# Performance work log

Measured on AMD Instinct MI355X. Metric: run time of the kernel, lower is better.

The kernel has to match this reference:

```python
import jax, jax.numpy as jnp
import numpy as np
from jax import lax

# Graph / problem sizes (a realistic chain denominator FST)
T, B, D = 150, 64, 2000   # frames, batch, num_pdfs
S, E = 3000, 100000       # FST states, FST arcs


def setup_inputs() -> dict:
    key = jax.random.key(0)
    k0, k1, k2, k3, k4, k5, k6 = jax.random.split(key, 7)
    inp = jax.random.normal(k0, (T, B, D), dtype=jnp.float32)          # nnet log-prob outputs
    from_state = jax.random.randint(k1, (E,), 0, S, dtype=jnp.int32)
    to_state = jax.random.randint(k2, (E,), 0, S, dtype=jnp.int32)
    pdf_id = jax.random.randint(k3, (E,), 0, D, dtype=jnp.int32)
    trans_logw = jax.random.normal(k4, (E,), dtype=jnp.float32) * 0.1 - 2.0  # arc log-weights
    init_logp = jax.random.normal(k5, (S,), dtype=jnp.float32) * 0.1 - np.log(S).astype(np.float32)
    final_logp = jax.random.normal(k6, (S,), dtype=jnp.float32) * 0.1 - 1.0
    return {
        "input": inp,
        "trans_logw": trans_logw,
        "init_logp": init_logp,
        "final_logp": final_logp,
        "from_state": from_state,
        "to_state": to_state,
        "pdf_id": pdf_id,
    }


def _logsumexp_scatter(scores, seg, num_segments):
    """Stable log-sum-exp of `scores` ([E, B]) scattered into segments along axis 0."""
    m = jax.ops.segment_max(scores, seg, num_segments=num_segments)      # [S, B]
    m_safe = jnp.where(jnp.isfinite(m), m, 0.0)
    s = jax.ops.segment_sum(jnp.exp(scores - m_safe[seg]), seg,
                            num_segments=num_segments)                   # [S, B]
    return jnp.where(s > 0, m_safe + jnp.log(s), -jnp.inf)


def reference(input, trans_logw, init_logp, final_logp, from_state, to_state, pdf_id):
    # Log-domain forward recursion over the denominator FST (LF-MMI denominator objf).
    # alpha: [S, B] log forward scores per state per sequence.
    num_states = init_logp.shape[0]
    alpha0 = jnp.broadcast_to(init_logp[:, None], (num_states, input.shape[1]))

    def step(alpha, x_t):
        # x_t: [B, D]. Arc score = alpha[src] + arc weight + emission log-prob of arc's pdf.
        scores = alpha[from_state] + trans_logw[:, None] + x_t.T[pdf_id]   # [E, B]
        alpha_next = _logsumexp_scatter(scores, to_state, num_states)      # [S, B]
        return alpha_next, None

    alpha_T, _ = lax.scan(step, alpha0, input)
    # Total log-likelihood: sum over batch of logsumexp over final states.
    objf = jnp.sum(jax.scipy.special.logsumexp(alpha_T + final_logp[:, None], axis=0))
    return objf
```

## Files before the change

### kernel.cpp

```cpp
#include <hip/hip_runtime.h>
#include <math.h>

#define TT 150
#define BB 64
#define DD 2000
#define SS 3000
#define EE 100000
#define EEPAD 124160
#define RESC 16
#define NSLOT 9
#define RESCC 0x1p-46f

#define NT 1024
#define NBLK 256
#define NG 16
#define GB 16
#define CAP 8192
#define ASTRD 3072
#define NSTMAX 1024
#define FLGSTR 32
#define NEXB 32
#define EXCH 125

#define OFF_ALPHA  0
#define OFF_EX     24064
#define OFF_ARC    40192
#define OFF_RBP    105728
#define OFF_SORD   109840
#define OFF_RED    113936
#define OFF_SH     118032
#define OFF_LSP    118048
#define DYNLDS     118128

struct __align__(8) ArcT2 { unsigned idx; float ew; };

__device__ inline float b2f(unsigned short u) {
    union { unsigned u32; float f; } x; x.u32 = ((unsigned)u) << 16; return x.f;
}
__device__ inline unsigned short f2b(float f) {
    union { float f; unsigned u; } x; x.f = f;
    unsigned r = x.u + 0x7FFF + ((x.u >> 16) & 1);
    return (unsigned short)(r >> 16);
}
__device__ inline float u2f(unsigned u) {
    union { unsigned u32; float f; } x; x.u32 = u; return x.f;
}

template <int CTRL>
__device__ inline float dpp_add(float v) {
    int x = __builtin_amdgcn_update_dpp(0, __float_as_int(v), CTRL, 0xF, 0xF, true);
    return v + __int_as_float(x);
}

__global__ void k_init0(int* __restrict__ counts, unsigned* __restrict__ flags,
                        float* __restrict__ partial)
{
    int i = blockIdx.x * blockDim.x + threadIdx.x;
    if (i < SS) counts[i] = 0;
    if (i < 2 * NBLK * FLGSTR) flags[i] = 0u;
    if (i < NG * 4) partial[i] = 0.f;
}

__global__ void k_zeroarcs(ArcT2* __restrict__ arcs)
{
    int i = blockIdx.x * blockDim.x + threadIdx.x;
    if (i < EEPAD) { ArcT2 z; z.idx = 0; z.ew = 0.f; arcs[i] = z; }
}

__global__ void k_hist(const int* __restrict__ to_state, int* __restrict__ counts)
{
    int e = blockIdx.x * blockDim.x + threadIdx.x;
    if (e < EE) atomicAdd(&counts[to_state[e]], 1);
}

__global__ void k_scan(const int* __restrict__ counts, int* __restrict__ rp,
                       int* __restrict__ cur)
{
    __shared__ int ls[1024];
    int tid = threadIdx.x;
    int s0 = tid * 3;
    int a0 = (s0 + 0 < SS) ? ((counts[s0 + 0] + 7) & ~7) : 0;
    int a1 = (s0 + 1 < SS) ? ((counts[s0 + 1] + 7) & ~7) : 0;
    int a2 = (s0 + 2 < SS) ? ((counts[s0 + 2] + 7) & ~7) : 0;
    int tsum = a0 + a1 + a2;
    ls[tid] = tsum;
    __syncthreads();
    for (int off = 1; off < 1024; off <<= 1) {
        int v = ls[tid];
        int add = (tid >= off) ? ls[tid - off] : 0;
        __syncthreads();
        ls[tid] = v + add;
        __syncthreads();
    }
    int excl = ls[tid] - tsum;
    if (s0 + 0 < SS) { rp[s0 + 0] = excl; cur[s0 + 0] = excl; }
    excl += a0;
    if (s0 + 1 < SS) { rp[s0 + 1] = excl; cur[s0 + 1] = excl; }
    excl += a1;
    if (s0 + 2 < SS) { rp[s0 + 2] = excl; cur[s0 + 2] = excl; }
    if (tid == 1023) rp[SS] = ls[1023];
}

__global__ void k_split(const int* __restrict__ rp, int* __restrict__ split)
{
    int j = threadIdx.x;
    if (j > GB) return;
    if (j == 0)  { split[0] = 0; return; }
    if (j == GB) { split[GB] = SS; return; }
    long long total = rp[SS];
    int target = (int)((total * j) / GB);
    int lo = 0, hi = SS;
    while (lo < hi) { int mid = (lo + hi) >> 1; if (rp[mid] >= target) hi = mid; else lo = mid + 1; }
    split[j] = lo;
}

__global__ void k_sortst(const int* __restrict__ rp, const int* __restrict__ split,
                         int* __restrict__ sordg)
{
    __shared__ int hist[128];
    __shared__ int off[128];
    int j = blockIdx.x;
    int s0 = split[j], s1 = split[j + 1];
    int nst = s1 - s0; if (nst > NSTMAX) nst = NSTMAX;
    int tid = threadIdx.x;
    if (tid < 128) hist[tid] = 0;
    __syncthreads();
    for (int i = tid; i < nst; i += 256) {
        int nit = (rp[s0 + i + 1] - rp[s0 + i]) >> 2;
        if (nit > 127) nit = 127;
        atomicAdd(&hist[nit], 1);
    }
    __syncthreads();
    if (tid == 0) {
        int acc = 0;
        for (int b = 127; b >= 0; --b) { off[b] = acc; acc += hist[b]; }
    }
    __syncthreads();
    for (int i = tid; i < nst; i += 256) {
        int nit = (rp[s0 + i + 1] - rp[s0 + i]) >> 2;
        if (nit > 127) nit = 127;
        int pos = atomicAdd(&off[nit], 1);
        sordg[j * NSTMAX + pos] = i;
    }
}

__global__ void k_scatter(const int* __restrict__ from_state, const int* __restrict__ to_state,
                          const int* __restrict__ pdf_id, const float* __restrict__ trans_logw,
                          int* __restrict__ cur, ArcT2* __restrict__ arcs)
{
    int e = blockIdx.x * blockDim.x + threadIdx.x;
    if (e >= EE) return;
    int s = to_state[e];
    int pos = atomicAdd(&cur[s], 1);
    ArcT2 a;
    a.idx = ((unsigned)from_state[e] << 3) | ((unsigned)pdf_id[e] << 19);
    a.ew = __expf(trans_logw[e]);
    arcs[pos] = a;
}

__global__ void __launch_bounds__(NT, 4) k_coop(
    const ArcT2* __restrict__ arcs, const int* __restrict__ rp,
    const int* __restrict__ split, const int* __restrict__ sordg,
    const float* __restrict__ input, const float* __restrict__ init_logp,
    const float* __restrict__ final_logp,
    float* __restrict__ partial,
    unsigned long long* __restrict__ A_all,
    unsigned* __restrict__ flags,
    unsigned* __restrict__ xcdbuf,
    float* __restrict__ out)
{
    extern __shared__ char dsm[];
    unsigned long long* la64  = (unsigned long long*)(dsm + OFF_ALPHA);
    unsigned long long* lex64 = (unsigned long long*)(dsm + OFF_EX);
    ArcT2*    larc  = (ArcT2*)(dsm + OFF_ARC);
    int*      rbp   = (int*)(dsm + OFF_RBP);
    float*    redf  = (float*)(dsm + OFF_RED);
    int*      sh    = (int*)(dsm + OFF_SH);
    int*      sord  = (int*)(dsm + OFF_SORD);
    int*      lsp   = (int*)(dsm + OFF_LSP);

    int tid = threadIdx.x, bid = blockIdx.x;
    int x = bid & 7, y = (bid >> 3) & 1, j = bid >> 4;
    int g = x * 2 + y;
    int lane = tid & 63, wave = tid >> 6;
    int qid = lane >> 2, sub = lane & 3;

    unsigned long long* Ag = A_all + (size_t)g * (2 * ASTRD);
    unsigned* stepf    = flags;
    unsigned* auxf     = flags + (size_t)NBLK * FLGSTR;
    unsigned* myflag   = stepf + (size_t)(g * GB + j) * FLGSTR;
    unsigned* grpflag  = stepf + (size_t)(g * GB) * FLGSTR;
    unsigned* myflag2  = auxf + (size_t)(g * GB + j) * FLGSTR;
    unsigned* grpflag2 = auxf + (size_t)(g * GB) * FLGSTR;
    const float* inpG  = input + (size_t)(4 * g) * DD;

    int s0 = split[j], s1 = split[j + 1];
    int nst = s1 - s0;
    if (nst > NSTMAX) nst = NSTMAX;

    for (int i = tid; i <= nst; i += NT) rbp[i] = rp[s0 + i];
    for (int i = tid; i < nst; i += NT) sord[i] = sordg[j * NSTMAX + i];
    if (tid <= GB) lsp[tid] = split[tid];
    __syncthreads();
    int rb0 = rbp[0];
    {
        int staged = rbp[nst] - rb0; if (staged > CAP) staged = CAP;
        for (int i = tid; i < staged; i += NT) larc[i] = arcs[rb0 + i];
    }

    unsigned xcd = __builtin_amdgcn_s_getreg(6164) & 0xF;
    if (tid == 0)
        __hip_atomic_store(&xcdbuf[g * GB + j], xcd, __ATOMIC_RELAXED, __HIP_MEMORY_SCOPE_AGENT);
    __syncthreads();
    if (tid == 0)
        __hip_atomic_store(myflag2, 1u, __ATOMIC_RELAXED, __HIP_MEMORY_SCOPE_AGENT);
    if (wave == 0) {
        while (true) {
            unsigned ok = 1;
            #pragma unroll
            for (int r = 0; r < 4; ++r) {
                unsigned v = __hip_atomic_load(auxf + (size_t)(lane * 4 + r) * FLGSTR,
                                               __ATOMIC_RELAXED, __HIP_MEMORY_SCOPE_AGENT);
                ok &= (v >= 1u);
            }
            if (__ballot(ok != 0) == ~0ULL) break;
            __builtin_amdgcn_s_sleep(1);
        }
    }
    __syncthreads();
    {
        int* xint = (int*)redf;
        if (tid < NBLK)
            xint[tid] = (int)__hip_atomic_load(&xcdbuf[tid], __ATOMIC_RELAXED,
                                               __HIP_MEMORY_SCOPE_AGENT);
        __syncthreads();
        if (tid == 0) {
            int x0 = xint[g * GB];
            int uni = 1;
            for (int m = 1; m < GB; ++m) uni &= (xint[g * GB + m] == x0);
            int first = xint[0], distinct = 0;
            for (int i = 1; i < NBLK; ++i) distinct |= (xint[i] != first);
            sh[0] = uni && distinct;
        }
        __syncthreads();
    }
    const bool fast = (sh[0] != 0);
    __syncthreads();

    float pf[2][4];
    auto prefetch = [&](const float* fr) {
        int d0 = wave * EXCH;
        #pragma unroll
        for (int r = 0; r < 2; ++r) {
            int dd = r * 64 + lane;
            if (dd < EXCH) {
                int d = d0 + dd;
                #pragma unroll
                for (int c = 0; c < 4; ++c) pf[r][c] = fr[c * DD + d];
            }
        }
    };

    auto exchange = [&](unsigned epv, const unsigned long long* src64) {
        {
            int d0 = wave * EXCH;
            #pragma unroll
            for (int r = 0; r < 2; ++r) {
                int dd = r * 64 + lane;
                if (dd < EXCH) {
                    int d = d0 + dd;
                    unsigned w0 = (unsigned)f2b(__expf(pf[r][0])) |
                                  ((unsigned)f2b(__expf(pf[r][1])) << 16);
                    unsigned w1 = (unsigned)f2b(__expf(pf[r][2])) |
                                  ((unsigned)f2b(__expf(pf[r][3])) << 16);
                    lex64[d] = (unsigned long long)w0 | ((unsigned long long)w1 << 32);
                }
            }
        }
        int p = wave;
        const unsigned* gf = grpflag + (size_t)p * FLGSTR;
        if (fast) {
            while (*(volatile const unsigned*)gf < epv) { }
            int a = lsp[p], b = lsp[p + 1];
            for (int i = a + lane; i < b; i += 64)
                la64[i] = *(volatile const unsigned long long*)(src64 + i);
        } else {
            while (__hip_atomic_load(gf, __ATOMIC_RELAXED, __HIP_MEMORY_SCOPE_AGENT) < epv)
                __builtin_amdgcn_s_sleep(1);
            int a = lsp[p], b = lsp[p + 1];
            for (int i = a + lane; i < b; i += 64)
                la64[i] = __hip_atomic_load(src64 + i, __ATOMIC_RELAXED,
                                            __HIP_MEMORY_SCOPE_AGENT);
        }
    };

    prefetch(inpG);
    for (int i = tid; i < nst; i += NT) {
        int s = s0 + i;
        unsigned short h = f2b(__expf(init_logp[s]));
        unsigned w = (unsigned)h | ((unsigned)h << 16);
        unsigned long long pk = (unsigned long long)w | ((unsigned long long)w << 32);
        if (fast) Ag[s] = pk;
        else __hip_atomic_store(Ag + s, pk, __ATOMIC_RELAXED, __HIP_MEMORY_SCOPE_AGENT);
    }
    __syncthreads();
    unsigned ep = 1;
    if (tid == 0) {
        if (fast) *(volatile unsigned*)myflag = ep;
        else __hip_atomic_store(myflag, ep, __ATOMIC_RELAXED, __HIP_MEMORY_SCOPE_AGENT);
    }
    exchange(ep, Ag );
    __syncthreads();

    float vf0 = 0.f, vf1 = 0.f, vf2 = 0.f, vf3 = 0.f;

    for (int k = 0; k < TT; ++k) {
        unsigned long long* An64 = Ag + ((k + 1) & 1) * ASTRD;
        bool last = (k == TT - 1);
        bool resc = (((k + 1) & (RESC - 1)) == 0);

        if (!last) prefetch(inpG + (size_t)(k + 1) * BB * DD);

        for (int base = wave * 16; base < nst; base += 256) {
            int li = base + qid;
            bool has = (li < nst);
            float acc0 = 0.f, acc1 = 0.f, acc2 = 0.f, acc3 = 0.f;
            int sg = 0;
            if (has) {
                int so = sord[li];
                sg = s0 + so;
                int ra = rbp[so], re = rbp[so + 1];
                int nit = (re - ra) >> 2;
                if (re - rb0 <= CAP) {
                    int bix = ra - rb0 + sub;
                    for (int t = 0; t < nit; ++t) {
                        ArcT2 a = larc[bix + t * 4];
                        uint2 au = *(const uint2*)(dsm + (a.idx & 0xFFFFu));
                        uint2 eu = *(const uint2*)(dsm + OFF_EX + (a.idx >> 16));
                        acc0 = fmaf(u2f(au.x << 16), a.ew * u2f(eu.x << 16), acc0);
                        acc1 = fmaf(u2f(au.x & 0xFFFF0000u), a.ew * u2f(eu.x & 0xFFFF0000u), acc1);
                        acc2 = fmaf(u2f(au.y << 16), a.ew * u2f(eu.y << 16), acc2);
                        acc3 = fmaf(u2f(au.y & 0xFFFF0000u), a.ew * u2f(eu.y & 0xFFFF0000u), acc3);
                    }
                } else {
                    for (int t = 0; t < nit; ++t) {
                        ArcT2 a = arcs[ra + t * 4 + sub];
                        uint2 au = *(const uint2*)(dsm + (a.idx & 0xFFFFu));
                        uint2 eu = *(const uint2*)(dsm + OFF_EX + (a.idx >> 16));
                        acc0 = fmaf(u2f(au.x << 16), a.ew * u2f(eu.x << 16), acc0);
                        acc1 = fmaf(u2f(au.x & 0xFFFF0000u), a.ew * u2f(eu.x & 0xFFFF0000u), acc1);
                        acc2 = fmaf(u2f(au.y << 16), a.ew * u2f(eu.y << 16), acc2);
                        acc3 = fmaf(u2f(au.y & 0xFFFF0000u), a.ew * u2f(eu.y & 0xFFFF0000u), acc3);
                    }
                }
            }
            acc0 = dpp_add<0xB1>(acc0); acc1 = dpp_add<0xB1>(acc1);
            acc2 = dpp_add<0xB1>(acc2); acc3 = dpp_add<0xB1>(acc3);
            acc0 = dpp_add<0x4E>(acc0); acc1 = dpp_add<0x4E>(acc1);
            acc2 = dpp_add<0x4E>(acc2); acc3 = dpp_add<0x4E>(acc3);
            if (has && sub == 0) {
                if (resc) { acc0 *= RESCC; acc1 *= RESCC; acc2 *= RESCC; acc3 *= RESCC; }
                if (last) {
                    float ef = __expf(final_logp[sg]);
                    vf0 = fmaf(acc0, ef, vf0);
                    vf1 = fmaf(acc1, ef, vf1);
                    vf2 = fmaf(acc2, ef, vf2);
                    vf3 = fmaf(acc3, ef, vf3);
                } else {
                    unsigned w0 = (unsigned)f2b(acc0) | ((unsigned)f2b(acc1) << 16);
                    unsigned w1 = (unsigned)f2b(acc2) | ((unsigned)f2b(acc3) << 16);
                    unsigned long long pk = (unsigned long long)w0 |
                                            ((unsigned long long)w1 << 32);
                    if (fast) An64[sg] = pk;
                    else __hip_atomic_store(An64 + sg, pk, __ATOMIC_RELAXED,
                                            __HIP_MEMORY_SCOPE_AGENT);
                }
            }
        }
        if (last) break;
        __syncthreads();
        ++ep;
        if (tid == 0) {
            if (fast) *(volatile unsigned*)myflag = ep;
            else __hip_atomic_store(myflag, ep, __ATOMIC_RELAXED, __HIP_MEMORY_SCOPE_AGENT);
        }
        exchange(ep, An64);
        __syncthreads();
    }

    if (sub == 0) {
        int r0 = (wave * 16 + qid) * 4;
        redf[r0 + 0] = vf0; redf[r0 + 1] = vf1;
        redf[r0 + 2] = vf2; redf[r0 + 3] = vf3;
    }
    __syncthreads();
    if (tid < 4) {
        float S = 0.f;
        for (int i = 0; i < 256; ++i) S += redf[i * 4 + tid];
        __hip_atomic_fetch_add(&partial[g * 4 + tid], S, __ATOMIC_RELAXED,
                               __HIP_MEMORY_SCOPE_AGENT);
    }
    __syncthreads();
    if (tid == 0)
        __hip_atomic_store(myflag2, 2u, __ATOMIC_RELAXED, __HIP_MEMORY_SCOPE_AGENT);
    if (j == 0) {
        if (wave == 0) {
            while (true) {
                unsigned v = 2;
                if (lane < GB)
                    v = __hip_atomic_load(grpflag2 + lane * FLGSTR, __ATOMIC_RELAXED,
                                          __HIP_MEMORY_SCOPE_AGENT);
                if (__ballot(v >= 2) == ~0ULL) break;
                __builtin_amdgcn_s_sleep(1);
            }
        }
        __syncthreads();
        if (tid < 4) {
            float S = __hip_atomic_load(&partial[g * 4 + tid], __ATOMIC_RELAXED,
                                        __HIP_MEMORY_SCOPE_AGENT);
            float lg = logf(S) + (float)(NSLOT * 46) * 0.69314718055994531f;
            atomicAdd(out, lg);
        }
    }
}

template <int THREADS>
__device__ inline void transpose_exp_t(const float* __restrict__ frame,
                                       unsigned short* __restrict__ dst,
                                       int tile_id, int tid, unsigned short* smem)
{
    int d0 = tile_id * 64;
    #pragma unroll
    for (int it = 0; it < 4096 / THREADS; ++it) {
        int idx = it * THREADS + tid;
        int dl = idx & 63, bl = idx >> 6;
        int d = d0 + dl;
        float v = 0.f;
        if (d < DD) v = __expf(frame[bl * DD + d]);
        smem[dl * 65 + bl] = f2b(v);
    }
    __syncthreads();
    #pragma unroll
    for (int it = 0; it < 4096 / THREADS; ++it) {
        int idx = it * THREADS + tid;
        int bo = idx & 63, dq = idx >> 6;
        int d = d0 + dq;
        if (d < DD) dst[(d << 6) + bo] = smem[dq * 65 + bo];
    }
    __syncthreads();
}

__global__ void k_initA(const float* __restrict__ init_logp,
                        unsigned short* __restrict__ A0, float* __restrict__ M2)
{
    int idx = blockIdx.x * blockDim.x + threadIdx.x;
    if (idx < SS * BB) A0[idx] = f2b(__expf(init_logp[idx >> 6]));
    if (idx < NSLOT * 16 * 64) M2[idx] = 0.f;
}

__global__ void k_transpose0(const float* __restrict__ frame, unsigned short* __restrict__ dst)
{
    __shared__ unsigned short tile[64 * 65];
    transpose_exp_t<256>(frame, dst, blockIdx.x, threadIdx.x, tile);
}

__global__ void __launch_bounds__(256) k_step(
    const ArcT2* __restrict__ arcs, const int* __restrict__ rp,
    const unsigned short* __restrict__ Ap, unsigned short* __restrict__ An,
    const unsigned short* __restrict__ ec,
    const float* __restrict__ frameNext, unsigned short* __restrict__ en,
    float* __restrict__ M2, int maxSlot, int useSlot)
{
    __shared__ unsigned short tile[64 * 65];
    __shared__ float part[256];
    __shared__ float rcpA[64];
    int tid = threadIdx.x, bid = blockIdx.x;
    if (bid >= SS) { transpose_exp_t<256>(frameNext, en, bid - SS, tid, tile); return; }
    int lane = tid & 63, wave = tid >> 6;
    if (useSlot >= 0 && wave == 0) {
        const float* Mrow = M2 + useSlot * (16 * 64);
        float m = Mrow[lane];
        #pragma unroll
        for (int g = 1; g < 16; ++g) m = fmaxf(m, Mrow[g * 64 + lane]);
        rcpA[lane] = 1.0f / m;
    }
    int rbeg = rp[bid], rend = rp[bid + 1];
    float acc = 0.f;
    for (int i = rbeg + wave; i < rend; i += 4) {
        ArcT2 a = arcs[i];
        int from = (a.idx & 0xFFFF) >> 3, pdf = a.idx >> 19;
        acc = fmaf(b2f(Ap[(from << 6) + lane]), a.ew * b2f(ec[(pdf << 6) + lane]), acc);
    }
    part[tid] = acc;
    __syncthreads();
    if (wave == 0) {
        float sum = part[lane] + part[64 + lane] + part[128 + lane] + part[192 + lane];
        if (useSlot >= 0) sum *= rcpA[lane];
        An[(bid << 6) + lane] = f2b(sum);
        if (maxSlot >= 0)
            atomicMax((unsigned*)&M2[maxSlot * (16 * 64) + (bid & 15) * 64 + lane],
                      __float_as_uint(sum));
    }
}

__global__ void k_fin(const unsigned short* __restrict__ AT, const float* __restrict__ final_logp,
                      const float* __restrict__ M2, float* __restrict__ out)
{
    __shared__ float red[1024];
    int tid = threadIdx.x;
    int lane = tid & 63, chunk = tid >> 6;
    float psum = 0.f;
    for (int s = chunk; s < SS; s += 16)
        psum += b2f(AT[(s << 6) + lane]) * __expf(final_logp[s]);
    red[tid] = psum;
    __syncthreads();
    if (tid < 64) {
        float sum = 0.f;
        #pragma unroll
        for (int c = 0; c < 16; ++c) sum += red[c * 64 + tid];
        float lg = logf(sum);
        #pragma unroll
        for (int r = 0; r < NSLOT; ++r) {
            const float* Mrow = M2 + r * (16 * 64);
            float m = Mrow[tid];
            #pragma unroll
            for (int g = 1; g < 16; ++g) m = fmaxf(m, Mrow[g * 64 + tid]);
            lg += logf(m);
        }
        #pragma unroll
        for (int off = 32; off > 0; off >>= 1) lg += __shfl_down(lg, off);
        if (tid == 0) out[0] = lg;
    }
}

extern "C" void kernel_launch(void* const* d_in, const int* in_sizes, int n_in,
                              void* d_out, int out_size, void* d_ws, size_t ws_size,
                              hipStream_t stream)
{
    const float* input      = (const float*)d_in[0];
    const float* trans_logw = (const float*)d_in[1];
    const float* init_logp  = (const float*)d_in[2];
    const float* final_logp = (const float*)d_in[3];
    const int*   from_state = (const int*)d_in[4];
    const int*   to_state   = (const int*)d_in[5];
    const int*   pdf_id     = (const int*)d_in[6];
    float* out = (float*)d_out;

    char* ws = (char*)d_ws;
    size_t off = 0;
    auto alloc = [&](size_t bytes) -> char* {
        char* p = ws + off;
        off = (off + bytes + 255) & ~(size_t)255;
        return p;
    };
    ArcT2* arcs  = (ArcT2*)alloc((size_t)EEPAD * sizeof(ArcT2));
    int* rp      = (int*)alloc((size_t)(SS + 1) * 4);
    int* cur     = (int*)alloc((size_t)SS * 4);
    int* counts  = (int*)alloc((size_t)SS * 4);
    int* split   = (int*)alloc((size_t)(GB + 1) * 4);
    int* sordg   = (int*)alloc((size_t)GB * NSTMAX * 4);
    unsigned long long* A_all = (unsigned long long*)alloc((size_t)NG * 2 * ASTRD * 8);
    float* partial  = (float*)alloc((size_t)NG * 4 * 4);
    unsigned* flags = (unsigned*)alloc((size_t)2 * NBLK * FLGSTR * 4);
    unsigned* xcdbuf = (unsigned*)alloc((size_t)NBLK * 4);
    unsigned short* A0  = (unsigned short*)alloc((size_t)SS * BB * 2);
    unsigned short* A1  = (unsigned short*)alloc((size_t)SS * BB * 2);
    unsigned short* EX0 = (unsigned short*)alloc((size_t)DD * BB * 2);
    unsigned short* EX1 = (unsigned short*)alloc((size_t)DD * BB * 2);
    float* M2    = (float*)alloc((size_t)NSLOT * 16 * 64 * 4);
    (void)ws_size; (void)in_sizes; (void)n_in; (void)out_size;

    k_init0<<<64, 256, 0, stream>>>(counts, flags, partial);
    k_zeroarcs<<<(EEPAD + 255) / 256, 256, 0, stream>>>(arcs);
    k_hist<<<(EE + 255) / 256, 256, 0, stream>>>(to_state, counts);
    k_scan<<<1, 1024, 0, stream>>>(counts, rp, cur);
    k_split<<<1, 32, 0, stream>>>(rp, split);
    k_sortst<<<GB, 256, 0, stream>>>(rp, split, sordg);
    k_scatter<<<(EE + 255) / 256, 256, 0, stream>>>(from_state, to_state, pdf_id,
                                                    trans_logw, cur, arcs);
    hipMemsetAsync(d_out, 0, sizeof(float), stream);

    hipFuncSetAttribute((const void*)k_coop, hipFuncAttributeMaxDynamicSharedMemorySize,
                        DYNLDS);
    int nb = 0;
    hipOccupancyMaxActiveBlocksPerMultiprocessor(&nb, (const void*)k_coop, NT, DYNLDS);
    if (nb >= 1) {
        void* kp[12] = {
            (void*)&arcs, (void*)&rp, (void*)&split, (void*)&sordg, (void*)&input,
            (void*)&init_logp, (void*)&final_logp, (void*)&partial, (void*)&A_all,
            (void*)&flags, (void*)&xcdbuf, (void*)&out
        };
        hipError_t e = hipLaunchCooperativeKernel((const void*)k_coop, dim3(NBLK), dim3(NT),
                                                  kp, DYNLDS, stream);
        if (e == hipSuccess) return;
    }

    k_initA<<<(SS * BB + 255) / 256, 256, 0, stream>>>(init_logp, A0, M2);
    k_transpose0<<<NEXB, 256, 0, stream>>>(input, EX0);
    unsigned short* A[2]  = {A0, A1};
    unsigned short* EX[2] = {EX0, EX1};
    for (int k = 0; k < TT; ++k) {
        int kn = k + 1;
        int useSlot = (k > 0 && (k % RESC) == 0) ? (k / RESC - 1) : -1;
        int maxSlot = (kn < TT && (kn % RESC) == 0) ? (kn / RESC - 1) : -1;
        int grid = SS + ((kn < TT) ? NEXB : 0);
        const float* fnext = (kn < TT) ? (input + (size_t)kn * BB * DD) : nullptr;
        k_step<<<grid, 256, 0, stream>>>(arcs, rp, A[k & 1], A[kn & 1], EX[k & 1],
                                         fnext, EX[kn & 1], M2, maxSlot, useSlot);
    }
    k_fin<<<1, 1024, 0, stream>>>(A[TT & 1], final_logp, M2, out);
}
```

Before: 640.0 us.

## Store alpha and emissions as fp32 in LDS, drop LDS arc staging

The LDS copies of alpha and the exponentiated emissions now hold unpacked fp32 float4 values instead of packed bf16, so the inner arc loop does plain float4 loads with no bit unpacking. To make room, the per-block staging of arcs into LDS is removed. Arcs are now read from global memory with a one-ahead software prefetch, and the arc index encoding is widened to 16-byte strides. This trades fewer ALU ops per arc for extra global/L2 traffic on arc records and doubled LDS bandwidth per gather.

```diff
diff --git a/kernel.cpp b/kernel.cpp
--- a/kernel.cpp
+++ b/kernel.cpp
@@ -15,7 +15,6 @@
 #define NBLK 256
 #define NG 16
 #define GB 16
-#define CAP 8192
 #define ASTRD 3072
 #define NSTMAX 1024
 #define FLGSTR 32
@@ -23,14 +22,13 @@
 #define EXCH 125
 
 #define OFF_ALPHA  0
-#define OFF_EX     24064
-#define OFF_ARC    40192
-#define OFF_RBP    105728
-#define OFF_SORD   109840
-#define OFF_RED    113936
-#define OFF_SH     118032
-#define OFF_LSP    118048
-#define DYNLDS     118128
+#define OFF_EX     48000
+#define OFF_RBP    80000
+#define OFF_SORD   84112
+#define OFF_RED    88208
+#define OFF_SH     92304
+#define OFF_LSP    92320
+#define DYNLDS     92400
 
 struct __align__(8) ArcT2 { unsigned idx; float ew; };
 
@@ -153,7 +151,7 @@
     int s = to_state[e];
     int pos = atomicAdd(&cur[s], 1);
     ArcT2 a;
-    a.idx = ((unsigned)from_state[e] << 3) | ((unsigned)pdf_id[e] << 19);
+    a.idx = ((unsigned)from_state[e] << 4) | ((unsigned)pdf_id[e] << 20);
     a.ew = __expf(trans_logw[e]);
     arcs[pos] = a;
 }
@@ -170,9 +168,8 @@
     float* __restrict__ out)
 {
     extern __shared__ char dsm[];
-    unsigned long long* la64  = (unsigned long long*)(dsm + OFF_ALPHA);
-    unsigned long long* lex64 = (unsigned long long*)(dsm + OFF_EX);
-    ArcT2*    larc  = (ArcT2*)(dsm + OFF_ARC);
+    float4*   laf4  = (float4*)(dsm + OFF_ALPHA);
+    float4*   lef4  = (float4*)(dsm + OFF_EX);
     int*      rbp   = (int*)(dsm + OFF_RBP);
     float*    redf  = (float*)(dsm + OFF_RED);
     int*      sh    = (int*)(dsm + OFF_SH);
@@ -201,12 +198,6 @@
     for (int i = tid; i <= nst; i += NT) rbp[i] = rp[s0 + i];
     for (int i = tid; i < nst; i += NT) sord[i] = sordg[j * NSTMAX + i];
     if (tid <= GB) lsp[tid] = split[tid];
-    __syncthreads();
-    int rb0 = rbp[0];
-    {
-        int staged = rbp[nst] - rb0; if (staged > CAP) staged = CAP;
-        for (int i = tid; i < staged; i += NT) larc[i] = arcs[rb0 + i];
-    }
 
     unsigned xcd = __builtin_amdgcn_s_getreg(6164) & 0xF;
     if (tid == 0)
@@ -269,11 +260,8 @@
                 int dd = r * 64 + lane;
                 if (dd < EXCH) {
                     int d = d0 + dd;
-                    unsigned w0 = (unsigned)f2b(__expf(pf[r][0])) |
-                                  ((unsigned)f2b(__expf(pf[r][1])) << 16);
-                    unsigned w1 = (unsigned)f2b(__expf(pf[r][2])) |
-                                  ((unsigned)f2b(__expf(pf[r][3])) << 16);
-                    lex64[d] = (unsigned long long)w0 | ((unsigned long long)w1 << 32);
+                    lef4[d] = make_float4(__expf(pf[r][0]), __expf(pf[r][1]),
+                                          __expf(pf[r][2]), __expf(pf[r][3]));
                 }
             }
         }
@@ -282,15 +270,23 @@
         if (fast) {
             while (*(volatile const unsigned*)gf < epv) { }
             int a = lsp[p], b = lsp[p + 1];
-            for (int i = a + lane; i < b; i += 64)
-                la64[i] = *(volatile const unsigned long long*)(src64 + i);
+            for (int i = a + lane; i < b; i += 64) {
+                unsigned long long v = *(volatile const unsigned long long*)(src64 + i);
+                unsigned lo = (unsigned)v, hi = (unsigned)(v >> 32);
+                laf4[i] = make_float4(u2f(lo << 16), u2f(lo & 0xFFFF0000u),
+                                      u2f(hi << 16), u2f(hi & 0xFFFF0000u));
+            }
         } else {
             while (__hip_atomic_load(gf, __ATOMIC_RELAXED, __HIP_MEMORY_SCOPE_AGENT) < epv)
                 __builtin_amdgcn_s_sleep(1);
             int a = lsp[p], b = lsp[p + 1];
-            for (int i = a + lane; i < b; i += 64)
-                la64[i] = __hip_atomic_load(src64 + i, __ATOMIC_RELAXED,
-                                            __HIP_MEMORY_SCOPE_AGENT);
+            for (int i = a + lane; i < b; i += 64) {
+                unsigned long long v = __hip_atomic_load(src64 + i, __ATOMIC_RELAXED,
+                                                         __HIP_MEMORY_SCOPE_AGENT);
+                unsigned lo = (unsigned)v, hi = (unsigned)(v >> 32);
+                laf4[i] = make_float4(u2f(lo << 16), u2f(lo & 0xFFFF0000u),
+                                      u2f(hi << 16), u2f(hi & 0xFFFF0000u));
+            }
         }
     };
 
@@ -331,26 +327,19 @@
                 sg = s0 + so;
                 int ra = rbp[so], re = rbp[so + 1];
                 int nit = (re - ra) >> 2;
-                if (re - rb0 <= CAP) {
-                    int bix = ra - rb0 + sub;
+                if (nit > 0) {
+                    int bix = ra + sub;
+                    ArcT2 a = arcs[bix];
                     for (int t = 0; t < nit; ++t) {
-                        ArcT2 a = larc[bix + t * 4];
-                        uint2 au = *(const uint2*)(dsm + (a.idx & 0xFFFFu));
-                        uint2 eu = *(const uint2*)(dsm + OFF_EX + (a.idx >> 16));
-                        acc0 = fmaf(u2f(au.x << 16), a.ew * u2f(eu.x << 16), acc0);
-                        acc1 = fmaf(u2f(au.x & 0xFFFF0000u), a.ew * u2f(eu.x & 0xFFFF0000u), acc1);
-                        acc2 = fmaf(u2f(au.y << 16), a.ew * u2f(eu.y << 16), acc2);
-                        acc3 = fmaf(u2f(au.y & 0xFFFF0000u), a.ew * u2f(eu.y & 0xFFFF0000u), acc3);
-                    }
-                } else {
-                    for (int t = 0; t < nit; ++t) {
-                        ArcT2 a = arcs[ra + t * 4 + sub];
-                        uint2 au = *(const uint2*)(dsm + (a.idx & 0xFFFFu));
-                        uint2 eu = *(const uint2*)(dsm + OFF_EX + (a.idx >> 16));
-                        acc0 = fmaf(u2f(au.x << 16), a.ew * u2f(eu.x << 16), acc0);
-                        acc1 = fmaf(u2f(au.x & 0xFFFF0000u), a.ew * u2f(eu.x & 0xFFFF0000u), acc1);
-                        acc2 = fmaf(u2f(au.y << 16), a.ew * u2f(eu.y << 16), acc2);
-                        acc3 = fmaf(u2f(au.y & 0xFFFF0000u), a.ew * u2f(eu.y & 0xFFFF0000u), acc3);
+                        ArcT2 an = arcs[bix + (t + 1) * 4];
+                        float4 al = *(const float4*)(dsm + (a.idx & 0xFFFFu));
+                        float4 ev = *(const float4*)(dsm + OFF_EX + (a.idx >> 16));
+                        float w = a.ew;
+                        acc0 = fmaf(al.x, w * ev.x, acc0);
+                        acc1 = fmaf(al.y, w * ev.y, acc1);
+                        acc2 = fmaf(al.z, w * ev.z, acc2);
+                        acc3 = fmaf(al.w, w * ev.w, acc3);
+                        a = an;
                     }
                 }
             }
@@ -488,7 +477,7 @@
     float acc = 0.f;
     for (int i = rbeg + wave; i < rend; i += 4) {
         ArcT2 a = arcs[i];
-        int from = (a.idx & 0xFFFF) >> 3, pdf = a.idx >> 19;
+        int from = (a.idx & 0xFFFF) >> 4, pdf = a.idx >> 20;
         acc = fmaf(b2f(Ap[(from << 6) + lane]), a.ew * b2f(ec[(pdf << 6) + lane]), acc);
     }
     part[tid] = acc;
```

Result: slower. 855.2 us (+33.6%).
